# Kernel optimization log

Hardware: AMD Instinct MI355X
Metric: run time of the kernel (lower is better)

## Reference

```python
import jax, jax.numpy as jnp
import numpy as np
import math

B, H, S, D = 2, 16, 2048, 64
NUM_BUCKETS = 32
MAX_DISTANCE = 128
TEMPERATURE = 8.0  # sqrt(D)
MASK_FILL = -1.0e9


def _relative_position_bucket(relative_position, num_buckets=NUM_BUCKETS, max_distance=MAX_DISTANCE):
    # bidirectional=True branch of the torch code
    num_buckets = num_buckets // 2
    n = -relative_position
    ret = (n < 0).astype(jnp.int32) * num_buckets
    n = jnp.abs(n)
    max_exact = num_buckets // 2
    is_small = n < max_exact
    val_if_large = max_exact + (
        jnp.log(n.astype(jnp.float32) / max_exact)
        / math.log(max_distance / max_exact)
        * (num_buckets - max_exact)
    ).astype(jnp.int32)
    val_if_large = jnp.minimum(val_if_large, num_buckets - 1)
    ret = ret + jnp.where(is_small, n, val_if_large)
    return ret


def setup_inputs() -> dict:
    key = jax.random.key(0)
    kq, kk, kv, kw, km = jax.random.split(key, 5)
    q = jax.random.normal(kq, (B, H, S, D), jnp.float32)
    k = jax.random.normal(kk, (B, H, S, D), jnp.float32)
    v = jax.random.normal(kv, (B, H, S, D), jnp.float32)
    bias_weight = jax.random.normal(kw, (NUM_BUCKETS, H), jnp.float32) * 0.02
    pos = jnp.broadcast_to(jnp.arange(S, dtype=jnp.int32)[None, :], (B, S))
    context_position = pos
    memory_position = pos
    mask = jax.random.randint(km, (B, 1, S, S), 0, 2) > 0  # bool, True = masked out
    return {
        'q': q, 'k': k, 'v': v, 'bias_weight': bias_weight,
        'context_position': context_position, 'memory_position': memory_position,
        'mask': mask,
    }


def reference(q, k, v, bias_weight, context_position, memory_position, mask):
    # attn scores: [B,H,S,S]
    attn = jnp.einsum('bhqd,bhkd->bhqk', q / TEMPERATURE, k)
    # T5-style relative position bias
    relative_position = memory_position[:, None, :] - context_position[:, :, None]  # [B,S,S]
    rp_bucket = _relative_position_bucket(relative_position)
    position_bias = bias_weight[rp_bucket]             # [B,S,S,H]
    position_bias = jnp.transpose(position_bias, (0, 3, 1, 2))  # [B,H,S,S]
    attn = attn + position_bias
    attn = jnp.where(mask, MASK_FILL, attn)
    attn = jax.nn.softmax(attn, axis=-1)  # dropout p=0.0 (eval) -> identity
    output = jnp.einsum('bhqk,bhkd->bhqd', attn, v)
    return output, attn, position_bias
```

## Files before the change

### kernel.cpp

```cpp
#include <hip/hip_runtime.h>
#include <math.h>

#define BB 2
#define HH 16
#define SS 2048
#define DD 64
#define TQ 8
#define FSTRIDE 2052
#define ERS 2056
#define ELO (8 * ERS)

typedef __attribute__((ext_vector_type(8))) short bf16x8;
typedef __attribute__((ext_vector_type(4))) float f32x4;
typedef __attribute__((ext_vector_type(4))) int i32x4;
typedef __attribute__((ext_vector_type(4))) unsigned short u16x4;

__device__ __forceinline__ unsigned short f2bf(float f) {
    unsigned u = __float_as_uint(f);
    u += 0x7FFF + ((u >> 16) & 1);
    return (unsigned short)(u >> 16);
}
__device__ __forceinline__ float bf2f(unsigned short h) {
    return __uint_as_float(((unsigned)h) << 16);
}

__device__ __forceinline__ int rel_bucket(int cpq, int mpk) {
    int n = cpq - mpk;
    int ret = 0;
    if (n < 0) { ret = 16; n = -n; }
    int v;
    if (n < 8) v = n;
    else {
        int j = (n >= 12) + (n >= 16) + (n >= 23) + (n >= 32) +
                (n >= 46) + (n >= 64) + (n >= 91);
        v = 8 + j;
    }
    return ret + v;
}

__launch_bounds__(256)
__global__ void conv_k_bf16(const float* __restrict__ src,
                            unsigned short* __restrict__ dst) {
    const size_t i = ((size_t)blockIdx.x * 256 + threadIdx.x) * 8;
    float4 f0 = *(const float4*)(src + i);
    float4 f1 = *(const float4*)(src + i + 4);
    union { bf16x8 v; unsigned short u[8]; } o;
    o.u[0] = f2bf(f0.x); o.u[1] = f2bf(f0.y); o.u[2] = f2bf(f0.z); o.u[3] = f2bf(f0.w);
    o.u[4] = f2bf(f1.x); o.u[5] = f2bf(f1.y); o.u[6] = f2bf(f1.z); o.u[7] = f2bf(f1.w);
    *(bf16x8*)(dst + i) = o.v;
}

__launch_bounds__(256)
__global__ void conv_v_t(const float* __restrict__ v,
                         unsigned short* __restrict__ vt_hi,
                         unsigned short* __restrict__ vt_lo) {
    __shared__ float tile[64][65];
    const int bh = blockIdx.x >> 5;
    const int ct = blockIdx.x & 31;
    const int c0 = ct * 64;
    const float* vb = v + ((size_t)bh * SS + c0) * DD;
    const int tid = threadIdx.x;
    #pragma unroll
    for (int it = 0; it < 16; ++it) {
        const int idx = it * 256 + tid;
        tile[idx >> 6][idx & 63] = vb[idx];
    }
    __syncthreads();
    #pragma unroll
    for (int it = 0; it < 16; ++it) {
        const int idx = it * 256 + tid;
        const int d = idx >> 6, c = idx & 63;
        const float val = tile[c][d];
        const unsigned short hi = f2bf(val);
        const unsigned short lo = f2bf(val - bf2f(hi));
        const size_t o = ((size_t)bh * DD + d) * SS + c0 + c;
        vt_hi[o] = hi;
        vt_lo[o] = lo;
    }
}

__launch_bounds__(512, 4)
__global__ void attn_tile_kernel(const float* __restrict__ qg,
                                 const unsigned short* __restrict__ kb,
                                 const unsigned short* __restrict__ vt_hi,
                                 const unsigned short* __restrict__ vt_lo,
                                 const float* __restrict__ bw,
                                 const int*   __restrict__ cp,
                                 const int*   __restrict__ mp,
                                 const int*   __restrict__ mask,
                                 float* __restrict__ o_out,
                                 float* __restrict__ a_out,
                                 float* __restrict__ p_out) {
    __shared__ __align__(16) unsigned short strip_sh[2 * 8 * ERS];
    __shared__ __align__(16) float partials[2 * TQ * DD];
    __shared__ __align__(16) unsigned short q_lds[16 * 72];
    __shared__ float bwh[32];
    __shared__ float invl[TQ];
    float* strip = (float*)strip_sh;

    const int tid = threadIdx.x;
    const int x   = blockIdx.x;
    const int xcd = x & 7;
    const int s_  = x >> 3;
    const int bh  = xcd * 4 + (s_ & 3);
    const int qt  = s_ >> 2;
    const int b   = bh >> 4;
    const int h   = bh & 15;
    const int q0  = qt * TQ;

    const unsigned short* Kbase = kb + (size_t)bh * SS * DD;

    {
        const float* Qrow = qg + ((size_t)bh * SS + q0) * DD;
        for (int e = tid; e < 16 * DD; e += 512) {
            int r = e >> 6, d = e & 63;
            q_lds[r * 72 + d] = (r < TQ) ? f2bf(Qrow[r * DD + d] * 0.125f)
                                         : (unsigned short)0;
        }
        if (tid < 32) bwh[tid] = bw[tid * HH + h];
    }
    __syncthreads();

    const int lane = tid & 63;
    const int wave = tid >> 6;
    const int quad = lane >> 4;
    const int l16  = lane & 15;

    {
        bf16x8 a0 = *(const bf16x8*)&q_lds[l16 * 72 + quad * 8];
        bf16x8 a1 = *(const bf16x8*)&q_lds[l16 * 72 + 32 + quad * 8];
        for (int ii = 0; ii < 16; ++ii) {
            const int kt = wave * 16 + ii;
            const unsigned short* kp = Kbase + (size_t)(kt * 16 + l16) * DD + quad * 8;
            bf16x8 b0 = *(const bf16x8*)(kp);
            bf16x8 b1 = *(const bf16x8*)(kp + 32);
            f32x4 acc = {0.f, 0.f, 0.f, 0.f};
            acc = __builtin_amdgcn_mfma_f32_16x16x32_bf16(a0, b0, acc, 0, 0, 0);
            acc = __builtin_amdgcn_mfma_f32_16x16x32_bf16(a1, b1, acc, 0, 0, 0);
            if (quad < 2) {
                const int col = kt * 16 + l16;
                const int rb  = quad * 4;
                strip[(rb + 0) * FSTRIDE + col] = acc[0];
                strip[(rb + 1) * FSTRIDE + col] = acc[1];
                strip[(rb + 2) * FSTRIDE + col] = acc[2];
                strip[(rb + 3) * FSTRIDE + col] = acc[3];
            }
        }
    }
    __syncthreads();

    {
        const int r  = wave;
        const int i  = lane;
        const int qi = q0 + r;
        const int cpq = cp[b * SS + qi];
        const int* mrow = mask + ((size_t)b * SS + qi) * SS;
        const int* mpb  = mp + b * SS;
        float* prow = p_out + ((size_t)bh * SS + qi) * SS;
        const float* srow = strip + r * FSTRIDE;
        float sv[32];
        float mx = -3.0e38f;
        #pragma unroll
        for (int j = 0; j < 8; ++j) {
            const int c0 = (i + 64 * j) * 4;
            i32x4 m4  = *(const i32x4*)(mrow + c0);
            i32x4 mp4 = *(const i32x4*)(mpb + c0);
            f32x4 s4  = *(const f32x4*)(srow + c0);
            f32x4 p4;
            #pragma unroll
            for (int u = 0; u < 4; ++u) {
                p4[u] = bwh[rel_bucket(cpq, mp4[u])];
                float s = s4[u] + p4[u];
                if (m4[u] != 0) s = -1.0e9f;
                sv[j * 4 + u] = s;
                mx = fmaxf(mx, s);
            }
            *(f32x4*)(prow + c0) = p4;
        }
        #pragma unroll
        for (int off = 32; off >= 1; off >>= 1)
            mx = fmaxf(mx, __shfl_xor(mx, off));

        __syncthreads();

        float sum = 0.f;
        #pragma unroll
        for (int j = 0; j < 32; ++j) {
            sv[j] = __expf(sv[j] - mx);
            sum += sv[j];
        }
        #pragma unroll
        for (int off = 32; off >= 1; off >>= 1)
            sum += __shfl_xor(sum, off);
        const float inv = 1.0f / sum;
        if (i == 0) invl[r] = inv;

        unsigned short* ehr = strip_sh + r * ERS;
        unsigned short* elr = strip_sh + ELO + r * ERS;
        float* arow = a_out + ((size_t)bh * SS + qi) * SS;
        #pragma unroll
        for (int j = 0; j < 8; ++j) {
            const int c0 = (i + 64 * j) * 4;
            f32x4 o4;
            u16x4 h4, l4;
            #pragma unroll
            for (int u = 0; u < 4; ++u) {
                const float e = sv[j * 4 + u];
                o4[u] = e * inv;
                const unsigned short hi = f2bf(e);
                h4[u] = hi;
                l4[u] = f2bf(e - bf2f(hi));
            }
            *(f32x4*)(arow + c0) = o4;
            *(u16x4*)(ehr + c0) = h4;
            *(u16x4*)(elr + c0) = l4;
        }
    }
    __syncthreads();

    {
        const int kc = wave >> 2;
        const int d0 = (wave & 3) * 16;
        const unsigned short* vhiB = vt_hi + ((size_t)bh * DD + d0 + l16) * SS;
        const unsigned short* vloB = vt_lo + ((size_t)bh * DD + d0 + l16) * SS;
        const unsigned short* ehB = strip_sh + (l16 & 7) * ERS + quad * 8;
        const unsigned short* elB = strip_sh + ELO + (l16 & 7) * ERS + quad * 8;
        f32x4 acc1 = {0.f, 0.f, 0.f, 0.f};
        f32x4 acc2 = {0.f, 0.f, 0.f, 0.f};
        f32x4 acc3 = {0.f, 0.f, 0.f, 0.f};
        #pragma unroll 4
        for (int s = 0; s < 32; ++s) {
            const int k0 = kc * 1024 + s * 32;
            bf16x8 ahi = *(const bf16x8*)(ehB + k0);
            bf16x8 alo = *(const bf16x8*)(elB + k0);
            bf16x8 bhi = *(const bf16x8*)(vhiB + k0 + quad * 8);
            bf16x8 blo = *(const bf16x8*)(vloB + k0 + quad * 8);
            acc1 = __builtin_amdgcn_mfma_f32_16x16x32_bf16(ahi, bhi, acc1, 0, 0, 0);
            acc2 = __builtin_amdgcn_mfma_f32_16x16x32_bf16(alo, bhi, acc2, 0, 0, 0);
            acc3 = __builtin_amdgcn_mfma_f32_16x16x32_bf16(ahi, blo, acc3, 0, 0, 0);
        }
        if (quad < 2) {
            #pragma unroll
            for (int rg = 0; rg < 4; ++rg) {
                const int row = quad * 4 + rg;
                partials[kc * (TQ * DD) + row * DD + d0 + l16] =
                    acc1[rg] + acc2[rg] + acc3[rg];
            }
        }
    }
    __syncthreads();

    {
        const int r = tid >> 6;
        const float v = partials[tid] + partials[512 + tid];
        o_out[((size_t)bh * SS + q0 + r) * DD + (tid & 63)] = v * invl[r];
    }
}

extern "C" void kernel_launch(void* const* d_in, const int* in_sizes, int n_in,
                              void* d_out, int out_size, void* d_ws, size_t ws_size,
                              hipStream_t stream) {
    const float* q  = (const float*)d_in[0];
    const float* k  = (const float*)d_in[1];
    const float* v  = (const float*)d_in[2];
    const float* bw = (const float*)d_in[3];
    const int*   cp = (const int*)d_in[4];
    const int*   mp = (const int*)d_in[5];
    const int*   mask = (const int*)d_in[6];

    float* o_out = (float*)d_out;
    float* a_out = o_out + (size_t)BB * HH * SS * DD;
    float* p_out = a_out + (size_t)BB * HH * SS * SS;

    const size_t NE = (size_t)BB * HH * SS * DD;
    unsigned short* kb    = (unsigned short*)d_ws;
    unsigned short* vt_hi = kb + NE;
    unsigned short* vt_lo = kb + 2 * NE;

    const int conv_grid = (int)(NE / (8 * 256));
    conv_k_bf16<<<conv_grid, 256, 0, stream>>>(k, kb);
    conv_v_t<<<BB * HH * (SS / 64), 256, 0, stream>>>(v, vt_hi, vt_lo);

    const int grid = BB * HH * (SS / TQ);
    attn_tile_kernel<<<grid, 512, 0, stream>>>(q, kb, vt_hi, vt_lo, bw, cp, mp, mask,
                                               o_out, a_out, p_out);
}
```

Measured before the change: 1.772 ms.

## Shrink LDS via chunked score buffer and re-read normalized probs from global

Replaces the full 8x2048 fp32 score strip with a double-buffered 256-column chunk buffer, so QK^T and the bias/mask pass are interleaved per chunk with a barrier each iteration. The PV stage now re-reads the just-written normalized attention rows from global memory and splits them into bf16 hi/lo with packed convert instructions, instead of keeping them in LDS. This removes the final 1/l rescale. Launch bounds are raised to 8 blocks per CU to exploit the smaller LDS footprint. The trade-off is extra global reads of the attention rows and more barriers, and the PV stage depends on those global writes being visible to the same block.

Result: slower. 2.394 ms (+35.1%).

```diff
diff --git a/kernel.cpp b/kernel.cpp
--- a/kernel.cpp
+++ b/kernel.cpp
@@ -6,14 +6,13 @@
 #define SS 2048
 #define DD 64
 #define TQ 8
-#define FSTRIDE 2052
-#define ERS 2056
-#define ELO (8 * ERS)
+#define CHUNK 256
+#define NCHUNK (SS / CHUNK)
+#define CSTR 264
 
 typedef __attribute__((ext_vector_type(8))) short bf16x8;
 typedef __attribute__((ext_vector_type(4))) float f32x4;
 typedef __attribute__((ext_vector_type(4))) int i32x4;
-typedef __attribute__((ext_vector_type(4))) unsigned short u16x4;
 
 __device__ __forceinline__ unsigned short f2bf(float f) {
     unsigned u = __float_as_uint(f);
@@ -22,6 +21,16 @@
 }
 __device__ __forceinline__ float bf2f(unsigned short h) {
     return __uint_as_float(((unsigned)h) << 16);
+}
+
+__device__ __forceinline__ void split2(float x0, float x1,
+                                       unsigned &hp, unsigned &lp) {
+    asm("v_cvt_pk_bf16_f32 %0, %1, %2" : "=v"(hp) : "v"(x0), "v"(x1));
+    const float h0 = __uint_as_float(hp << 16);
+    const float h1 = __uint_as_float(hp & 0xffff0000u);
+    const float l0 = x0 - h0;
+    const float l1 = x1 - h1;
+    asm("v_cvt_pk_bf16_f32 %0, %1, %2" : "=v"(lp) : "v"(l0), "v"(l1));
 }
 
 __device__ __forceinline__ int rel_bucket(int cpq, int mpk) {
@@ -79,7 +88,7 @@
     }
 }
 
-__launch_bounds__(512, 4)
+__launch_bounds__(512, 8)
 __global__ void attn_tile_kernel(const float* __restrict__ qg,
                                  const unsigned short* __restrict__ kb,
                                  const unsigned short* __restrict__ vt_hi,
@@ -91,12 +100,10 @@
                                  float* __restrict__ o_out,
                                  float* __restrict__ a_out,
                                  float* __restrict__ p_out) {
-    __shared__ __align__(16) unsigned short strip_sh[2 * 8 * ERS];
+    __shared__ __align__(16) float chunkbuf[2][TQ][CSTR];
     __shared__ __align__(16) float partials[2 * TQ * DD];
     __shared__ __align__(16) unsigned short q_lds[16 * 72];
     __shared__ float bwh[32];
-    __shared__ float invl[TQ];
-    float* strip = (float*)strip_sh;
 
     const int tid = threadIdx.x;
     const int x   = blockIdx.x;
@@ -126,63 +133,63 @@
     const int quad = lane >> 4;
     const int l16  = lane & 15;
 
-    {
-        bf16x8 a0 = *(const bf16x8*)&q_lds[l16 * 72 + quad * 8];
-        bf16x8 a1 = *(const bf16x8*)&q_lds[l16 * 72 + 32 + quad * 8];
-        for (int ii = 0; ii < 16; ++ii) {
-            const int kt = wave * 16 + ii;
-            const unsigned short* kp = Kbase + (size_t)(kt * 16 + l16) * DD + quad * 8;
-            bf16x8 b0 = *(const bf16x8*)(kp);
-            bf16x8 b1 = *(const bf16x8*)(kp + 32);
-            f32x4 acc = {0.f, 0.f, 0.f, 0.f};
-            acc = __builtin_amdgcn_mfma_f32_16x16x32_bf16(a0, b0, acc, 0, 0, 0);
-            acc = __builtin_amdgcn_mfma_f32_16x16x32_bf16(a1, b1, acc, 0, 0, 0);
-            if (quad < 2) {
-                const int col = kt * 16 + l16;
-                const int rb  = quad * 4;
-                strip[(rb + 0) * FSTRIDE + col] = acc[0];
-                strip[(rb + 1) * FSTRIDE + col] = acc[1];
-                strip[(rb + 2) * FSTRIDE + col] = acc[2];
-                strip[(rb + 3) * FSTRIDE + col] = acc[3];
+    const int r  = wave;
+    const int i  = lane;
+    const int qi = q0 + r;
+    const int cpq = cp[b * SS + qi];
+    const int* mrow = mask + ((size_t)b * SS + qi) * SS;
+    const int* mpb  = mp + b * SS;
+    float* prow = p_out + ((size_t)bh * SS + qi) * SS;
+    float sv[32];
+    float mx = -3.0e38f;
+
+    for (int c = 0; c < NCHUNK; ++c) {
+        {
+            bf16x8 a0 = *(const bf16x8*)&q_lds[l16 * 72 + quad * 8];
+            bf16x8 a1 = *(const bf16x8*)&q_lds[l16 * 72 + 32 + quad * 8];
+            #pragma unroll
+            for (int t = 0; t < 2; ++t) {
+                const int ktl = wave * 2 + t;
+                const int kt  = c * 16 + ktl;
+                const unsigned short* kp = Kbase + (size_t)(kt * 16 + l16) * DD + quad * 8;
+                bf16x8 b0 = *(const bf16x8*)(kp);
+                bf16x8 b1 = *(const bf16x8*)(kp + 32);
+                f32x4 acc = {0.f, 0.f, 0.f, 0.f};
+                acc = __builtin_amdgcn_mfma_f32_16x16x32_bf16(a0, b0, acc, 0, 0, 0);
+                acc = __builtin_amdgcn_mfma_f32_16x16x32_bf16(a1, b1, acc, 0, 0, 0);
+                if (quad < 2) {
+                    const int col = ktl * 16 + l16;
+                    const int rb  = quad * 4;
+                    chunkbuf[c & 1][rb + 0][col] = acc[0];
+                    chunkbuf[c & 1][rb + 1][col] = acc[1];
+                    chunkbuf[c & 1][rb + 2][col] = acc[2];
+                    chunkbuf[c & 1][rb + 3][col] = acc[3];
+                }
             }
         }
-    }
-    __syncthreads();
-
-    {
-        const int r  = wave;
-        const int i  = lane;
-        const int qi = q0 + r;
-        const int cpq = cp[b * SS + qi];
-        const int* mrow = mask + ((size_t)b * SS + qi) * SS;
-        const int* mpb  = mp + b * SS;
-        float* prow = p_out + ((size_t)bh * SS + qi) * SS;
-        const float* srow = strip + r * FSTRIDE;
-        float sv[32];
-        float mx = -3.0e38f;
-        #pragma unroll
-        for (int j = 0; j < 8; ++j) {
-            const int c0 = (i + 64 * j) * 4;
-            i32x4 m4  = *(const i32x4*)(mrow + c0);
-            i32x4 mp4 = *(const i32x4*)(mpb + c0);
-            f32x4 s4  = *(const f32x4*)(srow + c0);
+        __syncthreads();
+        {
+            const int cg = c * CHUNK + i * 4;
+            i32x4 m4  = *(const i32x4*)(mrow + cg);
+            i32x4 mp4 = *(const i32x4*)(mpb + cg);
+            f32x4 s4  = *(const f32x4*)&chunkbuf[c & 1][r][i * 4];
             f32x4 p4;
             #pragma unroll
             for (int u = 0; u < 4; ++u) {
                 p4[u] = bwh[rel_bucket(cpq, mp4[u])];
                 float s = s4[u] + p4[u];
                 if (m4[u] != 0) s = -1.0e9f;
-                sv[j * 4 + u] = s;
+                sv[c * 4 + u] = s;
                 mx = fmaxf(mx, s);
             }
-            *(f32x4*)(prow + c0) = p4;
-        }
+            *(f32x4*)(prow + cg) = p4;
+        }
+    }
+
+    {
         #pragma unroll
         for (int off = 32; off >= 1; off >>= 1)
             mx = fmaxf(mx, __shfl_xor(mx, off));
-
-        __syncthreads();
-
         float sum = 0.f;
         #pragma unroll
         for (int j = 0; j < 32; ++j) {
@@ -193,27 +200,14 @@
         for (int off = 32; off >= 1; off >>= 1)
             sum += __shfl_xor(sum, off);
         const float inv = 1.0f / sum;
-        if (i == 0) invl[r] = inv;
-
-        unsigned short* ehr = strip_sh + r * ERS;
-        unsigned short* elr = strip_sh + ELO + r * ERS;
         float* arow = a_out + ((size_t)bh * SS + qi) * SS;
         #pragma unroll
-        for (int j = 0; j < 8; ++j) {
-            const int c0 = (i + 64 * j) * 4;
+        for (int c = 0; c < NCHUNK; ++c) {
+            const int cg = c * CHUNK + i * 4;
             f32x4 o4;
-            u16x4 h4, l4;
-            #pragma unroll
-            for (int u = 0; u < 4; ++u) {
-                const float e = sv[j * 4 + u];
-                o4[u] = e * inv;
-                const unsigned short hi = f2bf(e);
-                h4[u] = hi;
-                l4[u] = f2bf(e - bf2f(hi));
-            }
-            *(f32x4*)(arow + c0) = o4;
-            *(u16x4*)(ehr + c0) = h4;
-            *(u16x4*)(elr + c0) = l4;
+            #pragma unroll
+            for (int u = 0; u < 4; ++u) o4[u] = sv[c * 4 + u] * inv;
+            *(f32x4*)(arow + cg) = o4;
         }
     }
     __syncthreads();
@@ -221,23 +215,27 @@
     {
         const int kc = wave >> 2;
         const int d0 = (wave & 3) * 16;
-        const unsigned short* vhiB = vt_hi + ((size_t)bh * DD + d0 + l16) * SS;
-        const unsigned short* vloB = vt_lo + ((size_t)bh * DD + d0 + l16) * SS;
-        const unsigned short* ehB = strip_sh + (l16 & 7) * ERS + quad * 8;
-        const unsigned short* elB = strip_sh + ELO + (l16 & 7) * ERS + quad * 8;
+        const float* aB = a_out + ((size_t)bh * SS + q0 + (l16 & 7)) * SS + quad * 8;
+        const unsigned short* vhiB = vt_hi + ((size_t)bh * DD + d0 + l16) * SS + quad * 8;
+        const unsigned short* vloB = vt_lo + ((size_t)bh * DD + d0 + l16) * SS + quad * 8;
         f32x4 acc1 = {0.f, 0.f, 0.f, 0.f};
         f32x4 acc2 = {0.f, 0.f, 0.f, 0.f};
         f32x4 acc3 = {0.f, 0.f, 0.f, 0.f};
-        #pragma unroll 4
+        #pragma unroll 2
         for (int s = 0; s < 32; ++s) {
             const int k0 = kc * 1024 + s * 32;
-            bf16x8 ahi = *(const bf16x8*)(ehB + k0);
-            bf16x8 alo = *(const bf16x8*)(elB + k0);
-            bf16x8 bhi = *(const bf16x8*)(vhiB + k0 + quad * 8);
-            bf16x8 blo = *(const bf16x8*)(vloB + k0 + quad * 8);
-            acc1 = __builtin_amdgcn_mfma_f32_16x16x32_bf16(ahi, bhi, acc1, 0, 0, 0);
-            acc2 = __builtin_amdgcn_mfma_f32_16x16x32_bf16(alo, bhi, acc2, 0, 0, 0);
-            acc3 = __builtin_amdgcn_mfma_f32_16x16x32_bf16(ahi, blo, acc3, 0, 0, 0);
+            f32x4 x0 = *(const f32x4*)(aB + k0);
+            f32x4 x1 = *(const f32x4*)(aB + k0 + 4);
+            union { bf16x8 v; unsigned u[4]; } ah, al;
+            split2(x0[0], x0[1], ah.u[0], al.u[0]);
+            split2(x0[2], x0[3], ah.u[1], al.u[1]);
+            split2(x1[0], x1[1], ah.u[2], al.u[2]);
+            split2(x1[2], x1[3], ah.u[3], al.u[3]);
+            bf16x8 bhi = *(const bf16x8*)(vhiB + k0);
+            bf16x8 blo = *(const bf16x8*)(vloB + k0);
+            acc1 = __builtin_amdgcn_mfma_f32_16x16x32_bf16(ah.v, bhi, acc1, 0, 0, 0);
+            acc2 = __builtin_amdgcn_mfma_f32_16x16x32_bf16(al.v, bhi, acc2, 0, 0, 0);
+            acc3 = __builtin_amdgcn_mfma_f32_16x16x32_bf16(ah.v, blo, acc3, 0, 0, 0);
         }
         if (quad < 2) {
             #pragma unroll
@@ -251,9 +249,9 @@
     __syncthreads();
 
     {
-        const int r = tid >> 6;
+        const int rr = tid >> 6;
         const float v = partials[tid] + partials[512 + tid];
-        o_out[((size_t)bh * SS + q0 + r) * DD + (tid & 63)] = v * invl[r];
+        o_out[((size_t)bh * SS + q0 + rr) * DD + (tid & 63)] = v;
     }
 }
 
```
